# Kernel optimization log

Hardware: AMD Instinct MI355X
Metric: run time of the kernel (lower is better)

The kernel has to match this reference:

```python
import jax, jax.numpy as jnp
import numpy as np

REL_SIZE = 65
TAG_SIZE = 4


def _rope(y):
    # Interleaved rotary position embedding, matching the torch module:
    # cos_pos = cos(theta) repeat_interleave(2), sin_pos = sin(theta) repeat_interleave(2)
    # y2 = (-y1, y0, -y3, y2, ...)
    B, S, H = y.shape
    half = H // 2
    pos = jnp.arange(S, dtype=jnp.float32)[:, None]                      # (S,1)
    inv_freq = jnp.power(10000.0, -2.0 * jnp.arange(half, dtype=jnp.float32) / H)
    theta = pos * inv_freq                                               # (S, half)
    cos = jnp.repeat(jnp.cos(theta), 2, axis=-1)                          # (S, H)
    sin = jnp.repeat(jnp.sin(theta), 2, axis=-1)                          # (S, H)
    yr = y.reshape(B, S, half, 2)
    y2 = jnp.stack([-yr[..., 1], yr[..., 0]], axis=-1).reshape(B, S, H)
    return y * cos + y2 * sin


def setup_inputs() -> dict:
    key = jax.random.key(0)
    k1, k2, k3 = jax.random.split(key, 3)
    B, S, H = 1, 160, 768
    y = jax.random.normal(k1, (B, S, H), dtype=jnp.float32)
    event_idx = jax.random.randint(k2, (B, 16), 0, S)
    W1 = jax.random.normal(k3, (H, 2 * H), dtype=jnp.float32) * 0.02
    b1 = jnp.zeros((H,), dtype=jnp.float32)
    W2 = jax.random.normal(jax.random.fold_in(key, 7), (REL_SIZE * TAG_SIZE, H), dtype=jnp.float32) * 0.02
    b2 = jnp.zeros((REL_SIZE * TAG_SIZE,), dtype=jnp.float32)
    return {"y": y, "event_idx": event_idx, "W1": W1, "b1": b1, "W2": W2, "b2": b2}


def reference(y, event_idx, W1, b1, W2, b2):
    # Eval path (training=False): event_idx unused, dropout = identity, sigmoid applied.
    B, S, H = y.shape
    yrot = _rope(y)
    # Linear(cat(a, b)) is separable: split W1 into the halves acting on a and b.
    Wa, Wb = W1[:, :H], W1[:, H:]
    left = jnp.einsum('bsh,oh->bso', yrot, Wa)                  # contribution of token i (row)
    right = jnp.einsum('bsh,oh->bso', yrot, Wb) + b1            # contribution of token j (col)
    h = jax.nn.relu(left[:, :, None, :] + right[:, None, :, :])  # (B, S, S, H)
    out = jnp.einsum('bijh,oh->bijo', h, W2) + b2               # (B, S, S, 260)
    out = out.reshape(B, S, S, REL_SIZE, TAG_SIZE).transpose(0, 3, 1, 2, 4)  # (B, 65, S, S, 4)
    return jax.nn.sigmoid(out)
```

## Files before the change

### kernel.cpp

```cpp
#include <hip/hip_runtime.h>
#include <hip/hip_bf16.h>
#include <cstdint>

#define SDIM 160
#define HDIM 768
#define HALF 384
#define ODIM 260
#define OPAD 272
#define CHUNK_BYTES 34816
#define WS_SMALL 1155088
#define WS_BIG   3514384

typedef __attribute__((ext_vector_type(8))) short short8;
typedef __attribute__((ext_vector_type(4))) float floatx4;

typedef const __attribute__((address_space(1))) unsigned char gl_u8;
typedef __attribute__((address_space(3))) unsigned char lds_u8;

static __device__ __forceinline__ float bf2f(unsigned short u) {
    union { unsigned int i; float f; } v; v.i = ((unsigned int)u) << 16; return v.f;
}
static __device__ __forceinline__ unsigned short f2bf(float x) {
    __hip_bfloat16 h = __float2bfloat16(x);
    return *reinterpret_cast<unsigned short*>(&h);
}
static __device__ __forceinline__ float q(float x) { return bf2f(f2bf(x)); }

__global__ __launch_bounds__(256) void prep_kernel(
    const float* __restrict__ y, const float* __restrict__ W1,
    const float* __restrict__ W2,
    unsigned short* __restrict__ yb, unsigned short* __restrict__ W2b,
    unsigned short* __restrict__ W1b, int do_w1b) {
    int bid = blockIdx.x;
    int t = threadIdx.x;
    if (bid < SDIM) {
        int s = bid;
        for (int p = t; p < HALF; p += 256) {
            float invf = __expf(-(2.0f * (float)p / (float)HDIM) * 9.210340371976184f);
            float th = (float)s * invf;
            float c = cosf(th), sn = sinf(th);
            float y0 = y[s * HDIM + 2 * p], y1 = y[s * HDIM + 2 * p + 1];
            yb[s * HDIM + 2 * p]     = f2bf(y0 * c - y1 * sn);
            yb[s * HDIM + 2 * p + 1] = f2bf(y1 * c + y0 * sn);
        }
    } else if (bid < SDIM + 102) {
        int idx = (bid - SDIM) * 256 + t;
        if (idx < 96 * OPAD) {
            int kg = idx % 96, row = idx / 96;
            unsigned short o8[8];
            if (row < ODIM) {
                float4 a = *reinterpret_cast<const float4*>(W2 + row * HDIM + kg * 8);
                float4 b = *reinterpret_cast<const float4*>(W2 + row * HDIM + kg * 8 + 4);
                o8[0] = f2bf(a.x); o8[1] = f2bf(a.y); o8[2] = f2bf(a.z); o8[3] = f2bf(a.w);
                o8[4] = f2bf(b.x); o8[5] = f2bf(b.y); o8[6] = f2bf(b.z); o8[7] = f2bf(b.w);
            } else {
                #pragma unroll
                for (int e = 0; e < 8; ++e) o8[e] = 0;
            }
            *reinterpret_cast<uint4*>(W2b + ((size_t)kg * OPAD + row) * 8) =
                *reinterpret_cast<uint4*>(o8);
        }
    } else if (do_w1b) {
        int idx = (bid - SDIM - 102) * 256 + t;
        int kg = idx % 96, row = idx / 96;
        const float* src = (row < 768) ? (W1 + row * 1536 + kg * 8)
                                       : (W1 + (row - 768) * 1536 + 768 + kg * 8);
        float4 a = *reinterpret_cast<const float4*>(src);
        float4 b = *reinterpret_cast<const float4*>(src + 4);
        unsigned short o8[8];
        o8[0] = f2bf(a.x); o8[1] = f2bf(a.y); o8[2] = f2bf(a.z); o8[3] = f2bf(a.w);
        o8[4] = f2bf(b.x); o8[5] = f2bf(b.y); o8[6] = f2bf(b.z); o8[7] = f2bf(b.w);
        *reinterpret_cast<uint4*>(W1b + ((size_t)kg * 1536 + row) * 8) =
            *reinterpret_cast<uint4*>(o8);
    }
}

__global__ __launch_bounds__(64, 2) void lr3_kernel(
    const unsigned short* __restrict__ yb, const unsigned short* __restrict__ W1b,
    const float* __restrict__ b1,
    unsigned short* __restrict__ Lb, unsigned short* __restrict__ Rb) {
    int l = threadIdx.x & 63;
    int l16 = l & 15, qd = l >> 4;
    int mtb = blockIdx.x * 4;
    int sp = blockIdx.y;
    int s0 = sp * 32 + l16;
    int s1 = s0 + 16;

    floatx4 acc[2][4];
    #pragma unroll
    for (int st = 0; st < 2; ++st)
        #pragma unroll
        for (int mtl = 0; mtl < 4; ++mtl)
            acc[st][mtl] = (floatx4){0.0f, 0.0f, 0.0f, 0.0f};

    const unsigned short* yrow0 = yb + s0 * HDIM;
    const unsigned short* yrow1 = yb + s1 * HDIM;

    for (int ks = 0; ks < 24; ++ks) {
        int k = ks * 32 + qd * 8;
        int kg = ks * 4 + qd;
        union { uint4 u; short8 s; } bu0, bu1;
        bu0.u = *reinterpret_cast<const uint4*>(yrow0 + k);
        bu1.u = *reinterpret_cast<const uint4*>(yrow1 + k);
        #pragma unroll
        for (int mtl = 0; mtl < 4; ++mtl) {
            union { uint4 u; short8 s; } au;
            au.u = *reinterpret_cast<const uint4*>(
                W1b + ((size_t)kg * 1536 + (mtb + mtl) * 16 + l16) * 8);
            acc[0][mtl] = __builtin_amdgcn_mfma_f32_16x16x32_bf16(
                au.s, bu0.s, acc[0][mtl], 0, 0, 0);
            acc[1][mtl] = __builtin_amdgcn_mfma_f32_16x16x32_bf16(
                au.s, bu1.s, acc[1][mtl], 0, 0, 0);
        }
    }

    #pragma unroll
    for (int st = 0; st < 2; ++st) {
        int s_out = sp * 32 + st * 16 + l16;
        #pragma unroll
        for (int mtl = 0; mtl < 4; ++mtl) {
            int o2 = (mtb + mtl) * 16 + qd * 4;
            unsigned short out4[4];
            if (o2 < 768) {
                #pragma unroll
                for (int r = 0; r < 4; ++r) out4[r] = f2bf(acc[st][mtl][r]);
                *reinterpret_cast<uint2*>(Lb + s_out * HDIM + o2) =
                    *reinterpret_cast<uint2*>(out4);
            } else {
                int ob = o2 - 768;
                #pragma unroll
                for (int r = 0; r < 4; ++r)
                    out4[r] = f2bf(acc[st][mtl][r] + b1[ob + r]);
                *reinterpret_cast<uint2*>(Rb + s_out * HDIM + ob) =
                    *reinterpret_cast<uint2*>(out4);
            }
        }
    }
}

__global__ __launch_bounds__(256) void lr_fallback_kernel(
    const unsigned short* __restrict__ yb, const float* __restrict__ W1,
    const float* __restrict__ b1,
    unsigned short* __restrict__ Lb, unsigned short* __restrict__ Rb) {
    int idx = blockIdx.x * 256 + threadIdx.x;
    int s = idx / 1536;
    int o2 = idx - s * 1536;
    const unsigned short* yrow = yb + s * HDIM;
    if (o2 < 768) {
        const float* wp = W1 + o2 * 1536;
        float a0 = 0.0f;
        for (int k = 0; k < HDIM; ++k) a0 += q(wp[k]) * bf2f(yrow[k]);
        Lb[s * HDIM + o2] = f2bf(a0);
    } else {
        int ob = o2 - 768;
        const float* wp = W1 + ob * 1536 + 768;
        float a0 = 0.0f;
        for (int k = 0; k < HDIM; ++k) a0 += q(wp[k]) * bf2f(yrow[k]);
        Rb[s * HDIM + ob] = f2bf(a0 + b1[ob]);
    }
}

__global__ __launch_bounds__(128, 3) void main_kernel(
    const unsigned short* __restrict__ Lb, const unsigned short* __restrict__ Rb,
    const unsigned short* __restrict__ W2b,
    const float* __restrict__ b2, float* __restrict__ out) {
    __shared__ __align__(16) unsigned char lds[CHUNK_BYTES];

    int w = threadIdx.x >> 6;
    int l = threadIdx.x & 63;
    int l16 = l & 15, qd = l >> 4;
    int mt0 = w * 9;
    int nmt = w ? 8 : 9;
    int i0 = blockIdx.x * 2;
    int j0 = blockIdx.y * 16;
    int j = j0 + l16;

    floatx4 acc[2][9];
    #pragma unroll
    for (int c = 0; c < 2; ++c)
        #pragma unroll
        for (int mtl = 0; mtl < 9; ++mtl)
            acc[c][mtl] = (floatx4){0.0f, 0.0f, 0.0f, 0.0f};

    const unsigned short* Lrow0 = Lb + i0 * HDIM;
    const unsigned short* Lrow1 = Lb + (i0 + 1) * HDIM;
    const unsigned short* Rrow  = Rb + j * HDIM;

    for (int kc = 0; kc < 12; ++kc) {
        __syncthreads();
        const unsigned char* gsrc =
            reinterpret_cast<const unsigned char*>(W2b) + kc * CHUNK_BYTES;
        #pragma unroll
        for (int it = 0; it < 17; ++it) {
            int off = (w * 17 + it) * 1024;
            __builtin_amdgcn_global_load_lds(
                (gl_u8*)(gsrc + off + l * 16),
                (lds_u8*)(lds + off),
                16, 0, 0);
        }
        __syncthreads();
        #pragma unroll
        for (int ks = 0; ks < 2; ++ks) {
            int k = kc * 64 + ks * 32 + qd * 8;
            short8 bfrag[2];
            #pragma unroll
            for (int c = 0; c < 2; ++c) {
                const unsigned short* Lr = c ? Lrow1 : Lrow0;
                union { uint4 u; unsigned short us[8]; } lu, ru;
                lu.u = *reinterpret_cast<const uint4*>(Lr + k);
                ru.u = *reinterpret_cast<const uint4*>(Rrow + k);
                short8 hb;
                #pragma unroll
                for (int e = 0; e < 8; ++e) {
                    float hv = bf2f(lu.us[e]) + bf2f(ru.us[e]);
                    hb[e] = (short)f2bf(fmaxf(hv, 0.0f));
                }
                bfrag[c] = hb;
            }
            int ldsbase = ((ks * 4 + qd) * OPAD + l16) * 16;
            #pragma unroll
            for (int mtl = 0; mtl < 9; ++mtl) {
                if (mtl < nmt) {
                    union { uint4 u; short8 s; } au;
                    au.u = *reinterpret_cast<const uint4*>(
                        lds + ldsbase + (mt0 + mtl) * 256);
                    acc[0][mtl] = __builtin_amdgcn_mfma_f32_16x16x32_bf16(
                        au.s, bfrag[0], acc[0][mtl], 0, 0, 0);
                    acc[1][mtl] = __builtin_amdgcn_mfma_f32_16x16x32_bf16(
                        au.s, bfrag[1], acc[1][mtl], 0, 0, 0);
                }
            }
        }
    }

    #pragma unroll
    for (int c = 0; c < 2; ++c) {
        int i = i0 + c;
        #pragma unroll
        for (int mtl = 0; mtl < 9; ++mtl) {
            if (mtl < nmt) {
                int ob = (mt0 + mtl) * 16 + qd * 4;
                if (ob < ODIM) {
                    float4 bv = *reinterpret_cast<const float4*>(b2 + ob);
                    int rel = ob >> 2;
                    float4 v;
                    v.x = 1.0f / (1.0f + __expf(-(acc[c][mtl][0] + bv.x)));
                    v.y = 1.0f / (1.0f + __expf(-(acc[c][mtl][1] + bv.y)));
                    v.z = 1.0f / (1.0f + __expf(-(acc[c][mtl][2] + bv.z)));
                    v.w = 1.0f / (1.0f + __expf(-(acc[c][mtl][3] + bv.w)));
                    *reinterpret_cast<float4*>(
                        out + (((rel * SDIM) + i) * SDIM + j) * 4) = v;
                }
            }
        }
    }
}

__global__ void ws_too_small_kernel(float* out) { out[0] = 999.0f; }

extern "C" void kernel_launch(void* const* d_in, const int* in_sizes, int n_in,
                              void* d_out, int out_size, void* d_ws, size_t ws_size,
                              hipStream_t stream) {
    const float* y  = (const float*)d_in[0];
    const float* W1 = (const float*)d_in[2];
    const float* b1 = (const float*)d_in[3];
    const float* W2 = (const float*)d_in[4];
    const float* b2 = (const float*)d_in[5];
    float* out = (float*)d_out;

    if (ws_size < (size_t)WS_SMALL) {
        ws_too_small_kernel<<<dim3(1), dim3(1), 0, stream>>>(out);
        return;
    }

    unsigned short* yb  = (unsigned short*)((char*)d_ws + 16);
    unsigned short* Lb  = yb + SDIM * HDIM;
    unsigned short* Rb  = Lb + SDIM * HDIM;
    unsigned short* W2b = Rb + SDIM * HDIM;
    unsigned short* W1b = W2b + 96 * OPAD * 8;

    if (ws_size >= (size_t)WS_BIG) {
        prep_kernel<<<dim3(SDIM + 102 + 576), dim3(256), 0, stream>>>(
            y, W1, W2, yb, W2b, W1b, 1);
        lr3_kernel<<<dim3(24, 5), dim3(64), 0, stream>>>(yb, W1b, b1, Lb, Rb);
        main_kernel<<<dim3(80, 10), dim3(128), 0, stream>>>(Lb, Rb, W2b, b2, out);
    } else {
        prep_kernel<<<dim3(SDIM + 102), dim3(256), 0, stream>>>(
            y, W1, W2, yb, W2b, W1b, 0);
        lr_fallback_kernel<<<dim3(960), dim3(256), 0, stream>>>(yb, W1, b1, Lb, Rb);
        main_kernel<<<dim3(80, 10), dim3(128), 0, stream>>>(Lb, Rb, W2b, b2, out);
    }
}
```

Baseline: 127.7 us.

## Switch pairwise hidden path to fp16 with packed add/relu and register-staged W2 prefetch

Stores L, R and W2 in fp16 instead of bf16 and uses the fp16 MFMA, so building the relu(L+R) fragment becomes packed half-precision adds and max ops rather than a per-element bf16-to-float-to-bf16 round trip. The W2 chunk loading moves from direct global-to-LDS loads to a register-staged prefetch: the next chunk is loaded into registers while the current one is computed, then written to LDS. Occupancy hint drops from 3 to 2 blocks per CU to fit the 17 extra uint4 registers. fp16 narrows the dynamic range compared with bf16, and the larger register footprint reduces occupancy.

```diff
diff --git a/kernel.cpp b/kernel.cpp
--- a/kernel.cpp
+++ b/kernel.cpp
@@ -13,15 +13,17 @@
 
 typedef __attribute__((ext_vector_type(8))) short short8;
 typedef __attribute__((ext_vector_type(4))) float floatx4;
-
-typedef const __attribute__((address_space(1))) unsigned char gl_u8;
-typedef __attribute__((address_space(3))) unsigned char lds_u8;
+typedef _Float16 half8 __attribute__((ext_vector_type(8)));
 
 static __device__ __forceinline__ float bf2f(unsigned short u) {
     union { unsigned int i; float f; } v; v.i = ((unsigned int)u) << 16; return v.f;
 }
 static __device__ __forceinline__ unsigned short f2bf(float x) {
     __hip_bfloat16 h = __float2bfloat16(x);
+    return *reinterpret_cast<unsigned short*>(&h);
+}
+static __device__ __forceinline__ unsigned short f2h(float x) {
+    _Float16 h = (_Float16)x;
     return *reinterpret_cast<unsigned short*>(&h);
 }
 static __device__ __forceinline__ float q(float x) { return bf2f(f2bf(x)); }
@@ -51,8 +53,8 @@
             if (row < ODIM) {
                 float4 a = *reinterpret_cast<const float4*>(W2 + row * HDIM + kg * 8);
                 float4 b = *reinterpret_cast<const float4*>(W2 + row * HDIM + kg * 8 + 4);
-                o8[0] = f2bf(a.x); o8[1] = f2bf(a.y); o8[2] = f2bf(a.z); o8[3] = f2bf(a.w);
-                o8[4] = f2bf(b.x); o8[5] = f2bf(b.y); o8[6] = f2bf(b.z); o8[7] = f2bf(b.w);
+                o8[0] = f2h(a.x); o8[1] = f2h(a.y); o8[2] = f2h(a.z); o8[3] = f2h(a.w);
+                o8[4] = f2h(b.x); o8[5] = f2h(b.y); o8[6] = f2h(b.z); o8[7] = f2h(b.w);
             } else {
                 #pragma unroll
                 for (int e = 0; e < 8; ++e) o8[e] = 0;
@@ -123,14 +125,14 @@
             unsigned short out4[4];
             if (o2 < 768) {
                 #pragma unroll
-                for (int r = 0; r < 4; ++r) out4[r] = f2bf(acc[st][mtl][r]);
+                for (int r = 0; r < 4; ++r) out4[r] = f2h(acc[st][mtl][r]);
                 *reinterpret_cast<uint2*>(Lb + s_out * HDIM + o2) =
                     *reinterpret_cast<uint2*>(out4);
             } else {
                 int ob = o2 - 768;
                 #pragma unroll
                 for (int r = 0; r < 4; ++r)
-                    out4[r] = f2bf(acc[st][mtl][r] + b1[ob + r]);
+                    out4[r] = f2h(acc[st][mtl][r] + b1[ob + r]);
                 *reinterpret_cast<uint2*>(Rb + s_out * HDIM + ob) =
                     *reinterpret_cast<uint2*>(out4);
             }
@@ -150,17 +152,17 @@
         const float* wp = W1 + o2 * 1536;
         float a0 = 0.0f;
         for (int k = 0; k < HDIM; ++k) a0 += q(wp[k]) * bf2f(yrow[k]);
-        Lb[s * HDIM + o2] = f2bf(a0);
+        Lb[s * HDIM + o2] = f2h(a0);
     } else {
         int ob = o2 - 768;
         const float* wp = W1 + ob * 1536 + 768;
         float a0 = 0.0f;
         for (int k = 0; k < HDIM; ++k) a0 += q(wp[k]) * bf2f(yrow[k]);
-        Rb[s * HDIM + ob] = f2bf(a0 + b1[ob]);
-    }
-}
-
-__global__ __launch_bounds__(128, 3) void main_kernel(
+        Rb[s * HDIM + ob] = f2h(a0 + b1[ob]);
+    }
+}
+
+__global__ __launch_bounds__(128, 2) void main_kernel(
     const unsigned short* __restrict__ Lb, const unsigned short* __restrict__ Rb,
     const unsigned short* __restrict__ W2b,
     const float* __restrict__ b2, float* __restrict__ out) {
@@ -186,48 +188,53 @@
     const unsigned short* Lrow1 = Lb + (i0 + 1) * HDIM;
     const unsigned short* Rrow  = Rb + j * HDIM;
 
+    const uint4* gv = reinterpret_cast<const uint4*>(W2b);
+    uint4* ldsv = reinterpret_cast<uint4*>(lds);
+
+    uint4 reg[17];
+    #pragma unroll
+    for (int it = 0; it < 17; ++it)
+        reg[it] = gv[it * 128 + threadIdx.x];
+
     for (int kc = 0; kc < 12; ++kc) {
         __syncthreads();
-        const unsigned char* gsrc =
-            reinterpret_cast<const unsigned char*>(W2b) + kc * CHUNK_BYTES;
-        #pragma unroll
-        for (int it = 0; it < 17; ++it) {
-            int off = (w * 17 + it) * 1024;
-            __builtin_amdgcn_global_load_lds(
-                (gl_u8*)(gsrc + off + l * 16),
-                (lds_u8*)(lds + off),
-                16, 0, 0);
-        }
+        #pragma unroll
+        for (int it = 0; it < 17; ++it)
+            ldsv[it * 128 + threadIdx.x] = reg[it];
         __syncthreads();
+        if (kc < 11) {
+            const uint4* gn = gv + (kc + 1) * 2176;
+            #pragma unroll
+            for (int it = 0; it < 17; ++it)
+                reg[it] = gn[it * 128 + threadIdx.x];
+        }
         #pragma unroll
         for (int ks = 0; ks < 2; ++ks) {
             int k = kc * 64 + ks * 32 + qd * 8;
-            short8 bfrag[2];
+            half8 bfrag[2];
             #pragma unroll
             for (int c = 0; c < 2; ++c) {
                 const unsigned short* Lr = c ? Lrow1 : Lrow0;
-                union { uint4 u; unsigned short us[8]; } lu, ru;
+                union { uint4 u; half8 h; } lu, ru;
                 lu.u = *reinterpret_cast<const uint4*>(Lr + k);
                 ru.u = *reinterpret_cast<const uint4*>(Rrow + k);
-                short8 hb;
+                half8 hv = lu.h + ru.h;
                 #pragma unroll
-                for (int e = 0; e < 8; ++e) {
-                    float hv = bf2f(lu.us[e]) + bf2f(ru.us[e]);
-                    hb[e] = (short)f2bf(fmaxf(hv, 0.0f));
-                }
-                bfrag[c] = hb;
+                for (int e = 0; e < 8; ++e)
+                    hv[e] = hv[e] > (_Float16)0.0f ? hv[e] : (_Float16)0.0f;
+                bfrag[c] = hv;
             }
             int ldsbase = ((ks * 4 + qd) * OPAD + l16) * 16;
             #pragma unroll
             for (int mtl = 0; mtl < 9; ++mtl) {
                 if (mtl < nmt) {
-                    union { uint4 u; short8 s; } au;
+                    union { uint4 u; half8 h; } au;
                     au.u = *reinterpret_cast<const uint4*>(
                         lds + ldsbase + (mt0 + mtl) * 256);
-                    acc[0][mtl] = __builtin_amdgcn_mfma_f32_16x16x32_bf16(
-                        au.s, bfrag[0], acc[0][mtl], 0, 0, 0);
-                    acc[1][mtl] = __builtin_amdgcn_mfma_f32_16x16x32_bf16(
-                        au.s, bfrag[1], acc[1][mtl], 0, 0, 0);
+                    acc[0][mtl] = __builtin_amdgcn_mfma_f32_16x16x32_f16(
+                        au.h, bfrag[0], acc[0][mtl], 0, 0, 0);
+                    acc[1][mtl] = __builtin_amdgcn_mfma_f32_16x16x32_f16(
+                        au.h, bfrag[1], acc[1][mtl], 0, 0, 0);
                 }
             }
         }
```

New measurement: 220.9 us. 73.0% more time.
